# Performance work log

Measured on AMD Instinct MI355X. Metric: run time of the kernel, lower is better.

Reference implementation:

```python
import jax, jax.numpy as jnp
import numpy as np

N = 50000
IN_F = 256
HID = 32
HEADS = 4
NEG_SLOPE = 0.2


def _gat_layer(x, edge_index, W, a_src, a_dst, bias):
    # x: [N, Fin]; W: [Fin, H*C]; a_src/a_dst: [H, C]; bias: [H*C]
    n = x.shape[0]
    H, C = a_src.shape
    h = (x @ W).reshape(n, H, C)                     # [N, H, C]
    alpha_src = jnp.einsum('nhc,hc->nh', h, a_src)   # [N, H]
    alpha_dst = jnp.einsum('nhc,hc->nh', h, a_dst)   # [N, H]
    src, dst = edge_index[0], edge_index[1]
    logits = alpha_src[src] + alpha_dst[dst]         # [E, H]
    logits = jax.nn.leaky_relu(logits, negative_slope=NEG_SLOPE)
    # segment softmax over edges grouped by destination node
    seg_max = jax.ops.segment_max(logits, dst, num_segments=n)
    seg_max = jnp.where(jnp.isfinite(seg_max), seg_max, 0.0)
    e = jnp.exp(logits - seg_max[dst])               # [E, H]
    denom = jax.ops.segment_sum(e, dst, num_segments=n)  # [N, H]
    attn = e / (denom[dst] + 1e-16)                  # [E, H]
    msg = h[src] * attn[:, :, None]                  # [E, H, C]
    out = jax.ops.segment_sum(msg, dst, num_segments=n)  # [N, H, C]
    return out.reshape(n, H * C) + bias


def _add_self_loops(edge_index, n):
    # PyG GATConv default add_self_loops=True
    loops = jnp.arange(n, dtype=edge_index.dtype)
    return jnp.concatenate([edge_index, jnp.stack([loops, loops])], axis=1)


def setup_inputs() -> dict:
    key = jax.random.key(0)
    ks = jax.random.split(key, 10)
    x = jax.random.normal(ks[0], (N, IN_F), dtype=jnp.float32)
    edge_index = jax.random.randint(ks[1], (2, 800000), 0, N, dtype=jnp.int64)
    d1 = HEADS * HID
    s1 = 1.0 / np.sqrt(IN_F)
    W1 = jax.random.normal(ks[2], (IN_F, d1), dtype=jnp.float32) * s1
    a_src1 = jax.random.normal(ks[3], (HEADS, HID), dtype=jnp.float32) * 0.1
    a_dst1 = jax.random.normal(ks[4], (HEADS, HID), dtype=jnp.float32) * 0.1
    b1 = jnp.zeros((d1,), dtype=jnp.float32)
    s2 = 1.0 / np.sqrt(d1)
    W2 = jax.random.normal(ks[5], (d1, d1), dtype=jnp.float32) * s2
    a_src2 = jax.random.normal(ks[6], (HEADS, HID), dtype=jnp.float32) * 0.1
    a_dst2 = jax.random.normal(ks[7], (HEADS, HID), dtype=jnp.float32) * 0.1
    b2 = jnp.zeros((d1,), dtype=jnp.float32)
    return {"x": x, "edge_index": edge_index, "W1": W1, "a_src1": a_src1,
            "a_dst1": a_dst1, "b1": b1, "W2": W2, "a_src2": a_src2,
            "a_dst2": a_dst2, "b2": b2}


def reference(x, edge_index, W1, a_src1, a_dst1, b1, W2, a_src2, a_dst2, b2):
    # Inference mode: dropout layers are identity.
    ei = _add_self_loops(edge_index, x.shape[0])
    h = _gat_layer(x, ei, W1, a_src1, a_dst1, b1)
    h = jax.nn.elu(h)
    h = _gat_layer(h, ei, W2, a_src2, a_dst2, b2)
    return h
```

## Files before the change

### kernel.cpp

```cpp
#include <hip/hip_runtime.h>
#include <hip/hip_fp16.h>
#include <math.h>

#define HEADS 4
#define HID 32
#define D1 128
#define IN_FEAT 256
#define NEG_SLOPE 0.2f
#define CAP 64
#define AGG_NODES 8
#define EPT 8

#define WTS_STRIDE_H 72
#define HTS_STRIDE_H 136
#define SMEM_BYTES (128 * 272)

typedef _Float16 half8 __attribute__((ext_vector_type(8)));
typedef float f32x4 __attribute__((ext_vector_type(4)));
typedef long long ll2 __attribute__((ext_vector_type(2)));

static inline int ceil_div(int a, int b) { return (a + b - 1) / b; }

static __device__ inline float2 unpack_h2(unsigned int v) {
    __half2 h = __builtin_bit_cast(__half2, v);
    return __half22float2(h);
}

static __device__ inline void fma_mix_lo(float& a, unsigned int h2, float w) {
    asm("v_fma_mix_f32 %0, %1, %2, %0 op_sel:[0,0,0] op_sel_hi:[1,0,0]"
        : "+v"(a) : "v"(h2), "v"(w));
}
static __device__ inline void fma_mix_hi(float& a, unsigned int h2, float w) {
    asm("v_fma_mix_f32 %0, %1, %2, %0 op_sel:[1,0,0] op_sel_hi:[1,0,0]"
        : "+v"(a) : "v"(h2), "v"(w));
}

__global__ void init_prep(const unsigned int* __restrict__ raw, int* __restrict__ flag,
                          const float* __restrict__ W1, _Float16* __restrict__ WT1,
                          const float* __restrict__ W2, _Float16* __restrict__ WT2,
                          int* __restrict__ cnt, int N) {
    int i = blockIdx.x * blockDim.x + threadIdx.x;
    if (i < N) cnt[i] = 0;
    if (i < IN_FEAT * D1) {
        int k = i >> 7, n = i & 127;
        WT1[(size_t)n * IN_FEAT + k] = (_Float16)W1[i];
    }
    if (i < D1 * D1) {
        int k = i >> 7, n = i & 127;
        WT2[(size_t)n * D1 + k] = (_Float16)W2[i];
    }
    if (blockIdx.x == 0 && threadIdx.x < 64) {
        unsigned int hi = raw[2 * threadIdx.x + 1];
        unsigned long long b = __ballot(hi != 0u);
        if (threadIdx.x == 0) *flag = (b == 0ULL) ? 1 : 0;
    }
}

__device__ void scatter_body(int sbid, const void* __restrict__ raw,
                             const int* __restrict__ flag,
                             int* __restrict__ cnt,
                             unsigned short* __restrict__ slots,
                             int E) {
    const int e0 = (sbid * 256 + (int)threadIdx.x) * EPT;
    if (e0 >= E) return;
    const bool wide = (*flag != 0);
    int s[EPT], d[EPT];
    if (e0 + EPT <= E) {
        if (wide) {
            const ll2* ps = (const ll2*)((const long long*)raw + e0);
            const ll2* pd = (const ll2*)((const long long*)raw + E + e0);
#pragma unroll
            for (int i = 0; i < EPT / 2; ++i) {
                ll2 a = ps[i], b = pd[i];
                s[2 * i] = (int)a[0]; s[2 * i + 1] = (int)a[1];
                d[2 * i] = (int)b[0]; d[2 * i + 1] = (int)b[1];
            }
        } else {
            const int4* ps = (const int4*)((const int*)raw + e0);
            const int4* pd = (const int4*)((const int*)raw + E + e0);
#pragma unroll
            for (int i = 0; i < EPT / 4; ++i) {
                int4 a = ps[i], b = pd[i];
                s[4 * i] = a.x; s[4 * i + 1] = a.y; s[4 * i + 2] = a.z; s[4 * i + 3] = a.w;
                d[4 * i] = b.x; d[4 * i + 1] = b.y; d[4 * i + 2] = b.z; d[4 * i + 3] = b.w;
            }
        }
        int p[EPT];
#pragma unroll
        for (int i = 0; i < EPT; ++i) p[i] = atomicAdd(&cnt[d[i]], 1);
#pragma unroll
        for (int i = 0; i < EPT; ++i)
            if (p[i] < CAP) slots[(size_t)d[i] * CAP + p[i]] = (unsigned short)s[i];
    } else {
        for (int e = e0; e < E; ++e) {
            int ss, dd;
            if (wide) { ss = (int)((const long long*)raw)[e]; dd = (int)((const long long*)raw)[E + e]; }
            else      { ss = ((const int*)raw)[e];            dd = ((const int*)raw)[E + e]; }
            int p = atomicAdd(&cnt[dd], 1);
            if (p < CAP) slots[(size_t)dd * CAP + p] = (unsigned short)ss;
        }
    }
}

template <int AF16>
__device__ void gemm_body(char* smem, int bid, const void* __restrict__ Ain,
                          const _Float16* __restrict__ WT,
                          _Float16* __restrict__ Hout,
                          const float* __restrict__ a_src,
                          const float* __restrict__ a_dst,
                          float* __restrict__ asrc_out,
                          float* __restrict__ adst_out,
                          int M, int K) {
    const int tid = threadIdx.x;
    const int wave = tid >> 6, lane = tid & 63;
    const int quad = lane >> 4, l16 = lane & 15;
    const int row0 = bid * 128;
    const int m0 = min(row0 + wave * 32 + l16, M - 1);
    const int m1 = min(row0 + wave * 32 + 16 + l16, M - 1);
    const float*    Af = (const float*)Ain;
    const _Float16* Ah = (const _Float16*)Ain;
    const uint4* WTg = (const uint4*)WT;
    const int K8 = K >> 3;

    f32x4 acc[2][8];
#pragma unroll
    for (int r = 0; r < 2; ++r)
#pragma unroll
        for (int c = 0; c < 8; ++c) acc[r][c] = (f32x4){0.f, 0.f, 0.f, 0.f};

    for (int kb = 0; kb < K; kb += 64) {
        __syncthreads();
#pragma unroll
        for (int i = 0; i < 4; ++i) {
            int c = tid + i * 256;
            int n = c >> 3, j = c & 7;
            uint4 v = WTg[(size_t)n * K8 + (kb >> 3) + j];
            *(uint4*)(smem + n * 144 + j * 16) = v;
        }
        __syncthreads();
#pragma unroll
        for (int kc = 0; kc < 2; ++kc) {
            int k0 = kb + kc * 32 + quad * 8;
            half8 a0f, a1f;
            if (AF16) {
                a0f = *(const half8*)(Ah + (size_t)m0 * K + k0);
                a1f = *(const half8*)(Ah + (size_t)m1 * K + k0);
            } else {
                float4 x0 = *(const float4*)(Af + (size_t)m0 * K + k0);
                float4 x1 = *(const float4*)(Af + (size_t)m0 * K + k0 + 4);
                float4 y0 = *(const float4*)(Af + (size_t)m1 * K + k0);
                float4 y1 = *(const float4*)(Af + (size_t)m1 * K + k0 + 4);
                a0f[0] = (_Float16)x0.x; a0f[1] = (_Float16)x0.y;
                a0f[2] = (_Float16)x0.z; a0f[3] = (_Float16)x0.w;
                a0f[4] = (_Float16)x1.x; a0f[5] = (_Float16)x1.y;
                a0f[6] = (_Float16)x1.z; a0f[7] = (_Float16)x1.w;
                a1f[0] = (_Float16)y0.x; a1f[1] = (_Float16)y0.y;
                a1f[2] = (_Float16)y0.z; a1f[3] = (_Float16)y0.w;
                a1f[4] = (_Float16)y1.x; a1f[5] = (_Float16)y1.y;
                a1f[6] = (_Float16)y1.z; a1f[7] = (_Float16)y1.w;
            }
#pragma unroll
            for (int c = 0; c < 8; ++c) {
                half8 bf = *(const half8*)(smem + (c * 16 + l16) * 144 + kc * 64 + quad * 16);
                acc[0][c] = __builtin_amdgcn_mfma_f32_16x16x32_f16(a0f, bf, acc[0][c], 0, 0, 0);
                acc[1][c] = __builtin_amdgcn_mfma_f32_16x16x32_f16(a1f, bf, acc[1][c], 0, 0, 0);
            }
        }
    }

    __syncthreads();
    _Float16* hts = (_Float16*)smem;
#pragma unroll
    for (int r = 0; r < 2; ++r)
#pragma unroll
        for (int c = 0; c < 8; ++c)
#pragma unroll
            for (int g = 0; g < 4; ++g) {
                int row = wave * 32 + r * 16 + quad * 4 + g;
                hts[row * HTS_STRIDE_H + c * 16 + l16] = (_Float16)acc[r][c][g];
            }
    __syncthreads();

    const int r = tid >> 1;
    const int part = tid & 1;
    const int grow = row0 + r;
    const uint4* hrow = (const uint4*)(smem + r * 272 + part * 128);
    if (grow < M) {
        uint4* dv = (uint4*)(Hout + (size_t)grow * 128 + part * 64);
#pragma unroll
        for (int i = 0; i < 8; ++i) dv[i] = hrow[i];
    }
#pragma unroll
    for (int t = 0; t < 2; ++t) {
        int hh = part * 2 + t;
        const uint4* hv = (const uint4*)(smem + r * 272 + hh * 64);
        const float4* as4 = (const float4*)(a_src + hh * HID);
        const float4* ad4 = (const float4*)(a_dst + hh * HID);
        float ps = 0.f, pd = 0.f;
#pragma unroll
        for (int b = 0; b < 4; ++b) {
            uint4 u = hv[b];
            float2 f0 = unpack_h2(u.x), f1 = unpack_h2(u.y);
            float2 f2 = unpack_h2(u.z), f3 = unpack_h2(u.w);
            float4 s0 = as4[b * 2], s1 = as4[b * 2 + 1];
            float4 d0 = ad4[b * 2], d1 = ad4[b * 2 + 1];
            ps += f0.x * s0.x + f0.y * s0.y + f1.x * s0.z + f1.y * s0.w
                + f2.x * s1.x + f2.y * s1.y + f3.x * s1.z + f3.y * s1.w;
            pd += f0.x * d0.x + f0.y * d0.y + f1.x * d0.z + f1.y * d0.w
                + f2.x * d1.x + f2.y * d1.y + f3.x * d1.z + f3.y * d1.w;
        }
        if (grow < M) {
            asrc_out[grow * 4 + hh] = ps;
            adst_out[grow * 4 + hh] = pd;
        }
    }
}

template <int AF16>
__global__ __launch_bounds__(256) void gemm128(const void* __restrict__ Ain,
                                               const _Float16* __restrict__ WT,
                                               _Float16* __restrict__ Hout,
                                               const float* __restrict__ a_src,
                                               const float* __restrict__ a_dst,
                                               float* __restrict__ asrc_out,
                                               float* __restrict__ adst_out,
                                               int M, int K) {
    __shared__ __align__(16) char smem[SMEM_BYTES];
    gemm_body<AF16>(smem, blockIdx.x, Ain, WT, Hout, a_src, a_dst,
                    asrc_out, adst_out, M, K);
}

template <int AF16>
__global__ __launch_bounds__(256) void gemm128_scatter(const void* __restrict__ Ain,
                                                       const _Float16* __restrict__ WT,
                                                       _Float16* __restrict__ Hout,
                                                       const float* __restrict__ a_src,
                                                       const float* __restrict__ a_dst,
                                                       float* __restrict__ asrc_out,
                                                       float* __restrict__ adst_out,
                                                       int M, int K,
                                                       const void* __restrict__ raw,
                                                       const int* __restrict__ flag,
                                                       int* __restrict__ cnt,
                                                       unsigned short* __restrict__ slots,
                                                       int E, int Sg) {
    __shared__ __align__(16) char smem[SMEM_BYTES];
    if ((int)blockIdx.x < Sg) {
        scatter_body(blockIdx.x, raw, flag, cnt, slots, E);
        return;
    }
    gemm_body<AF16>(smem, blockIdx.x - Sg, Ain, WT, Hout, a_src, a_dst,
                    asrc_out, adst_out, M, K);
}

__global__ __launch_bounds__(256) void aggregate(const _Float16* __restrict__ hb,
                                                 const int* __restrict__ cnt,
                                                 const unsigned short* __restrict__ slots,
                                                 const float* __restrict__ asrc,
                                                 const float* __restrict__ adst,
                                                 const float* __restrict__ bias,
                                                 float* __restrict__ out32,
                                                 _Float16* __restrict__ out16,
                                                 int N, int apply_elu) {
    const int w = threadIdx.x >> 6;
    const int lane = threadIdx.x & 63;
    const int half = lane >> 5;
    const int hl = lane & 31;
    const int idx = w * 2 + half;
    const int node = blockIdx.x * AGG_NODES + idx;
    const bool live = (node < N);

    __shared__ float wsh[AGG_NODES][CAP][4];
    __shared__ int ssh[AGG_NODES][CAP];

    int cntE = 0, count = 1;
    if (live) {
        cntE = min(cnt[node], CAP - 1);
        count = cntE + 1;
    }
    const unsigned short* nslots = slots + (size_t)node * CAP;

    float4 ad4 = live ? *(const float4*)&adst[node * 4] : make_float4(0.f, 0.f, 0.f, 0.f);

    const bool v0 = live && (hl < count);
    const bool v1 = live && (hl + 32 < count);
    float lv0[4] = {-1e30f, -1e30f, -1e30f, -1e30f};
    float lv1[4] = {-1e30f, -1e30f, -1e30f, -1e30f};
    if (v0) {
        int src = (hl < cntE) ? (int)nslots[hl] : node;
        ssh[idx][hl] = src << 8;
        float4 as4 = *(const float4*)&asrc[src * 4];
        float t0 = as4.x + ad4.x, t1 = as4.y + ad4.y;
        float t2 = as4.z + ad4.z, t3 = as4.w + ad4.w;
        lv0[0] = t0 > 0.f ? t0 : NEG_SLOPE * t0;
        lv0[1] = t1 > 0.f ? t1 : NEG_SLOPE * t1;
        lv0[2] = t2 > 0.f ? t2 : NEG_SLOPE * t2;
        lv0[3] = t3 > 0.f ? t3 : NEG_SLOPE * t3;
    }
    if (v1) {
        int j = hl + 32;
        int src = (j < cntE) ? (int)nslots[j] : node;
        ssh[idx][j] = src << 8;
        float4 as4 = *(const float4*)&asrc[src * 4];
        float t0 = as4.x + ad4.x, t1 = as4.y + ad4.y;
        float t2 = as4.z + ad4.z, t3 = as4.w + ad4.w;
        lv1[0] = t0 > 0.f ? t0 : NEG_SLOPE * t0;
        lv1[1] = t1 > 0.f ? t1 : NEG_SLOPE * t1;
        lv1[2] = t2 > 0.f ? t2 : NEG_SLOPE * t2;
        lv1[3] = t3 > 0.f ? t3 : NEG_SLOPE * t3;
    }

    float m[4];
#pragma unroll
    for (int h = 0; h < 4; ++h) m[h] = fmaxf(lv0[h], lv1[h]);
#pragma unroll
    for (int off = 16; off >= 1; off >>= 1)
#pragma unroll
        for (int h = 0; h < 4; ++h)
            m[h] = fmaxf(m[h], __shfl_xor(m[h], off, 64));

    float e0[4], e1[4], sum[4];
#pragma unroll
    for (int h = 0; h < 4; ++h) {
        e0[h] = v0 ? __expf(lv0[h] - m[h]) : 0.f;
        e1[h] = v1 ? __expf(lv1[h] - m[h]) : 0.f;
        sum[h] = e0[h] + e1[h];
    }
#pragma unroll
    for (int off = 16; off >= 1; off >>= 1)
#pragma unroll
        for (int h = 0; h < 4; ++h)
            sum[h] += __shfl_xor(sum[h], off, 64);

    if (v0) {
        float4 w4;
        w4.x = e0[0] / (sum[0] + 1e-16f);
        w4.y = e0[1] / (sum[1] + 1e-16f);
        w4.z = e0[2] / (sum[2] + 1e-16f);
        w4.w = e0[3] / (sum[3] + 1e-16f);
        *(float4*)&wsh[idx][hl][0] = w4;
    }
    if (v1) {
        float4 w4;
        w4.x = e1[0] / (sum[0] + 1e-16f);
        w4.y = e1[1] / (sum[1] + 1e-16f);
        w4.z = e1[2] / (sum[2] + 1e-16f);
        w4.w = e1[3] / (sum[3] + 1e-16f);
        *(float4*)&wsh[idx][hl + 32][0] = w4;
    }
    __syncthreads();

    const int q = hl >> 4;
    const int sub = hl & 15;
    const int hh = sub >> 2;
    const char* hbase = (const char*)hb;
    const int sub16 = sub * 16;

    float acc[8];
#pragma unroll
    for (int i = 0; i < 8; ++i) acc[i] = 0.f;

#define LDROW(off) (*(const uint4*)(hbase + (unsigned)((off) + sub16)))
#define ROW_FMA(u, wt)                                   \
    do {                                                 \
        fma_mix_lo(acc[0], (u).x, (wt));                 \
        fma_mix_hi(acc[1], (u).x, (wt));                 \
        fma_mix_lo(acc[2], (u).y, (wt));                 \
        fma_mix_hi(acc[3], (u).y, (wt));                 \
        fma_mix_lo(acc[4], (u).z, (wt));                 \
        fma_mix_hi(acc[5], (u).z, (wt));                 \
        fma_mix_lo(acc[6], (u).w, (wt));                 \
        fma_mix_hi(acc[7], (u).w, (wt));                 \
    } while (0)

    if (live) {
        int j = q;
        if (j + 6 < count) {
            int o0 = ssh[idx][j], o1 = ssh[idx][j + 2], o2 = ssh[idx][j + 4], o3 = ssh[idx][j + 6];
            float w0 = wsh[idx][j][hh], w1 = wsh[idx][j + 2][hh];
            float w2 = wsh[idx][j + 4][hh], w3 = wsh[idx][j + 6][hh];
            uint4 u0 = LDROW(o0), u1 = LDROW(o1), u2 = LDROW(o2), u3 = LDROW(o3);
            for (j += 8; j + 6 < count; j += 8) {
                int p0 = ssh[idx][j], p1 = ssh[idx][j + 2], p2 = ssh[idx][j + 4], p3 = ssh[idx][j + 6];
                float x0 = wsh[idx][j][hh], x1 = wsh[idx][j + 2][hh];
                float x2 = wsh[idx][j + 4][hh], x3 = wsh[idx][j + 6][hh];
                uint4 n0 = LDROW(p0), n1 = LDROW(p1), n2 = LDROW(p2), n3 = LDROW(p3);
                ROW_FMA(u0, w0); ROW_FMA(u1, w1); ROW_FMA(u2, w2); ROW_FMA(u3, w3);
                u0 = n0; u1 = n1; u2 = n2; u3 = n3;
                w0 = x0; w1 = x1; w2 = x2; w3 = x3;
            }
            const bool b0 = j < count, b1 = j + 2 < count, b2 = j + 4 < count;
            uint4 t0 = {0, 0, 0, 0}, t1 = {0, 0, 0, 0}, t2 = {0, 0, 0, 0};
            float y0 = 0.f, y1 = 0.f, y2 = 0.f;
            if (b0) { t0 = LDROW(ssh[idx][j]);     y0 = wsh[idx][j][hh]; }
            if (b1) { t1 = LDROW(ssh[idx][j + 2]); y1 = wsh[idx][j + 2][hh]; }
            if (b2) { t2 = LDROW(ssh[idx][j + 4]); y2 = wsh[idx][j + 4][hh]; }
            ROW_FMA(u0, w0); ROW_FMA(u1, w1); ROW_FMA(u2, w2); ROW_FMA(u3, w3);
            if (b0) ROW_FMA(t0, y0);
            if (b1) ROW_FMA(t1, y1);
            if (b2) ROW_FMA(t2, y2);
        } else {
            const bool b0 = j < count, b1 = j + 2 < count, b2 = j + 4 < count;
            uint4 t0 = {0, 0, 0, 0}, t1 = {0, 0, 0, 0}, t2 = {0, 0, 0, 0};
            float y0 = 0.f, y1 = 0.f, y2 = 0.f;
            if (b0) { t0 = LDROW(ssh[idx][j]);     y0 = wsh[idx][j][hh]; }
            if (b1) { t1 = LDROW(ssh[idx][j + 2]); y1 = wsh[idx][j + 2][hh]; }
            if (b2) { t2 = LDROW(ssh[idx][j + 4]); y2 = wsh[idx][j + 4][hh]; }
            if (b0) ROW_FMA(t0, y0);
            if (b1) ROW_FMA(t1, y1);
            if (b2) ROW_FMA(t2, y2);
        }
    }
#undef ROW_FMA
#undef LDROW

#pragma unroll
    for (int i = 0; i < 8; ++i) acc[i] += __shfl_xor(acc[i], 16, 64);

    if (live && q == 0) {
        int ch8 = sub * 8;
        float o[8];
#pragma unroll
        for (int i = 0; i < 8; ++i) o[i] = acc[i] + bias[ch8 + i];
        if (apply_elu) {
#pragma unroll
            for (int i = 0; i < 8; ++i) o[i] = o[i] > 0.f ? o[i] : __expf(o[i]) - 1.f;
        }
        if (out16) {
            __align__(16) _Float16 t[8];
#pragma unroll
            for (int i = 0; i < 8; ++i) t[i] = (_Float16)o[i];
            *(uint4*)&out16[(size_t)node * D1 + ch8] = *(const uint4*)t;
        } else {
            *(float4*)&out32[(size_t)node * D1 + ch8]     = make_float4(o[0], o[1], o[2], o[3]);
            *(float4*)&out32[(size_t)node * D1 + ch8 + 4] = make_float4(o[4], o[5], o[6], o[7]);
        }
    }
}

extern "C" void kernel_launch(void* const* d_in, const int* in_sizes, int n_in,
                              void* d_out, int out_size, void* d_ws, size_t ws_size,
                              hipStream_t stream) {
    const float* x      = (const float*)d_in[0];
    const void*  e_raw  = d_in[1];
    const float* W1     = (const float*)d_in[2];
    const float* a_src1 = (const float*)d_in[3];
    const float* a_dst1 = (const float*)d_in[4];
    const float* b1     = (const float*)d_in[5];
    const float* W2     = (const float*)d_in[6];
    const float* a_src2 = (const float*)d_in[7];
    const float* a_dst2 = (const float*)d_in[8];
    const float* b2     = (const float*)d_in[9];

    const int N  = in_sizes[0] / IN_FEAT;
    const int E  = in_sizes[1] / 2;
    float* out = (float*)d_out;

    char* ws = (char*)d_ws;
    size_t woff = 0;
    auto walloc = [&](size_t bytes) -> char* {
        char* p = ws + woff;
        woff = (woff + bytes + 255) & ~(size_t)255;
        return p;
    };
    int*   flag  = (int*)walloc(4);
    int*   cnt   = (int*)walloc((size_t)N * 4);
    unsigned short* slots = (unsigned short*)walloc((size_t)N * CAP * 2);
    float* asrc  = (float*)walloc((size_t)N * HEADS * 4);
    float* adst  = (float*)walloc((size_t)N * HEADS * 4);
    _Float16* hb  = (_Float16*)walloc((size_t)N * D1 * 2);
    _Float16* o16 = (_Float16*)walloc((size_t)N * D1 * 2);
    _Float16* WT1 = (_Float16*)walloc((size_t)IN_FEAT * D1 * 2);
    _Float16* WT2 = (_Float16*)walloc((size_t)D1 * D1 * 2);

    const int Gg = ceil_div(N, 128);
    const int Sg = ceil_div(E, 256 * EPT);
    const int Ga = ceil_div(N, AGG_NODES);
    const int initN = (N > IN_FEAT * D1) ? N : IN_FEAT * D1;

    init_prep<<<ceil_div(initN, 256), 256, 0, stream>>>(
        (const unsigned int*)e_raw, flag, W1, WT1, W2, WT2, cnt, N);
    gemm128_scatter<0><<<Sg + Gg, 256, 0, stream>>>(
        x, WT1, hb, a_src1, a_dst1, asrc, adst, N, IN_FEAT,
        e_raw, flag, cnt, slots, E, Sg);
    aggregate<<<Ga, 256, 0, stream>>>(hb, cnt, slots, asrc, adst, b1, nullptr, o16, N, 1);
    gemm128<1><<<Gg, 256, 0, stream>>>(o16, WT2, hb, a_src2, a_dst2, asrc, adst, N, D1);
    aggregate<<<Ga, 256, 0, stream>>>(hb, cnt, slots, asrc, adst, b2, out, nullptr, N, 0);
}
```

Baseline: 244.2 us.

## Fuse all GAT stages into one persistent cooperative kernel with grid syncs

Replaces the five separate kernel launches (init, gemm+scatter, aggregate, gemm, aggregate) with a single persistent cooperative kernel that loops over virtual blocks and separates stages with grid-wide syncs. The goal is to remove launch overhead and inter-kernel gaps. The cost is that grid size is capped by occupancy, so each stage runs as grid-stride loops with one shared-memory allocation sized for the GEMM. Grid barriers add their own cost. The previous multi-launch path is kept as a fallback if the cooperative launch fails.

```diff
diff --git a/kernel.cpp b/kernel.cpp
--- a/kernel.cpp
+++ b/kernel.cpp
@@ -1,6 +1,9 @@
 #include <hip/hip_runtime.h>
 #include <hip/hip_fp16.h>
+#include <hip/hip_cooperative_groups.h>
 #include <math.h>
+
+namespace cg = cooperative_groups;
 
 #define HEADS 4
 #define HID 32
@@ -14,6 +17,7 @@
 #define WTS_STRIDE_H 72
 #define HTS_STRIDE_H 136
 #define SMEM_BYTES (128 * 272)
+#define AGG_SMEM (AGG_NODES * CAP * 4 * 4 + AGG_NODES * CAP * 4)
 
 typedef _Float16 half8 __attribute__((ext_vector_type(8)));
 typedef float f32x4 __attribute__((ext_vector_type(4)));
@@ -33,27 +37,6 @@
 static __device__ inline void fma_mix_hi(float& a, unsigned int h2, float w) {
     asm("v_fma_mix_f32 %0, %1, %2, %0 op_sel:[1,0,0] op_sel_hi:[1,0,0]"
         : "+v"(a) : "v"(h2), "v"(w));
-}
-
-__global__ void init_prep(const unsigned int* __restrict__ raw, int* __restrict__ flag,
-                          const float* __restrict__ W1, _Float16* __restrict__ WT1,
-                          const float* __restrict__ W2, _Float16* __restrict__ WT2,
-                          int* __restrict__ cnt, int N) {
-    int i = blockIdx.x * blockDim.x + threadIdx.x;
-    if (i < N) cnt[i] = 0;
-    if (i < IN_FEAT * D1) {
-        int k = i >> 7, n = i & 127;
-        WT1[(size_t)n * IN_FEAT + k] = (_Float16)W1[i];
-    }
-    if (i < D1 * D1) {
-        int k = i >> 7, n = i & 127;
-        WT2[(size_t)n * D1 + k] = (_Float16)W2[i];
-    }
-    if (blockIdx.x == 0 && threadIdx.x < 64) {
-        unsigned int hi = raw[2 * threadIdx.x + 1];
-        unsigned long long b = __ballot(hi != 0u);
-        if (threadIdx.x == 0) *flag = (b == 0ULL) ? 1 : 0;
-    }
 }
 
 __device__ void scatter_body(int sbid, const void* __restrict__ raw,
@@ -216,62 +199,26 @@
     }
 }
 
-template <int AF16>
-__global__ __launch_bounds__(256) void gemm128(const void* __restrict__ Ain,
-                                               const _Float16* __restrict__ WT,
-                                               _Float16* __restrict__ Hout,
-                                               const float* __restrict__ a_src,
-                                               const float* __restrict__ a_dst,
-                                               float* __restrict__ asrc_out,
-                                               float* __restrict__ adst_out,
-                                               int M, int K) {
-    __shared__ __align__(16) char smem[SMEM_BYTES];
-    gemm_body<AF16>(smem, blockIdx.x, Ain, WT, Hout, a_src, a_dst,
-                    asrc_out, adst_out, M, K);
-}
-
-template <int AF16>
-__global__ __launch_bounds__(256) void gemm128_scatter(const void* __restrict__ Ain,
-                                                       const _Float16* __restrict__ WT,
-                                                       _Float16* __restrict__ Hout,
-                                                       const float* __restrict__ a_src,
-                                                       const float* __restrict__ a_dst,
-                                                       float* __restrict__ asrc_out,
-                                                       float* __restrict__ adst_out,
-                                                       int M, int K,
-                                                       const void* __restrict__ raw,
-                                                       const int* __restrict__ flag,
-                                                       int* __restrict__ cnt,
-                                                       unsigned short* __restrict__ slots,
-                                                       int E, int Sg) {
-    __shared__ __align__(16) char smem[SMEM_BYTES];
-    if ((int)blockIdx.x < Sg) {
-        scatter_body(blockIdx.x, raw, flag, cnt, slots, E);
-        return;
-    }
-    gemm_body<AF16>(smem, blockIdx.x - Sg, Ain, WT, Hout, a_src, a_dst,
-                    asrc_out, adst_out, M, K);
-}
-
-__global__ __launch_bounds__(256) void aggregate(const _Float16* __restrict__ hb,
-                                                 const int* __restrict__ cnt,
-                                                 const unsigned short* __restrict__ slots,
-                                                 const float* __restrict__ asrc,
-                                                 const float* __restrict__ adst,
-                                                 const float* __restrict__ bias,
-                                                 float* __restrict__ out32,
-                                                 _Float16* __restrict__ out16,
-                                                 int N, int apply_elu) {
+__device__ void agg_body(char* smem_, int bid,
+                         const _Float16* __restrict__ hb,
+                         const int* __restrict__ cnt,
+                         const unsigned short* __restrict__ slots,
+                         const float* __restrict__ asrc,
+                         const float* __restrict__ adst,
+                         const float* __restrict__ bias,
+                         float* __restrict__ out32,
+                         _Float16* __restrict__ out16,
+                         int N, int apply_elu) {
+    float (*wsh)[CAP][4] = (float (*)[CAP][4])smem_;
+    int (*ssh)[CAP] = (int (*)[CAP])(smem_ + AGG_NODES * CAP * 4 * sizeof(float));
+
     const int w = threadIdx.x >> 6;
     const int lane = threadIdx.x & 63;
     const int half = lane >> 5;
     const int hl = lane & 31;
     const int idx = w * 2 + half;
-    const int node = blockIdx.x * AGG_NODES + idx;
+    const int node = bid * AGG_NODES + idx;
     const bool live = (node < N);
-
-    __shared__ float wsh[AGG_NODES][CAP][4];
-    __shared__ int ssh[AGG_NODES][CAP];
 
     int cntE = 0, count = 1;
     if (live) {
@@ -436,6 +383,133 @@
             *(float4*)&out32[(size_t)node * D1 + ch8 + 4] = make_float4(o[4], o[5], o[6], o[7]);
         }
     }
+    __syncthreads();
+}
+
+struct MegaArgs {
+    const void* x; const void* e_raw;
+    const float *W1, *as1, *ad1, *b1, *W2, *as2, *ad2, *b2;
+    int* flag; int* cnt; unsigned short* slots;
+    float *asrc, *adst;
+    _Float16 *hb, *o16, *WT1, *WT2;
+    float* out;
+    int N, E, initN, Sg, Gg, Ga;
+};
+
+__global__ __launch_bounds__(256) void mega(MegaArgs a) {
+    __shared__ __align__(16) char smem[SMEM_BYTES];
+    cg::grid_group grid = cg::this_grid();
+
+    for (int i = blockIdx.x * 256 + (int)threadIdx.x; i < a.initN; i += gridDim.x * 256) {
+        if (i < a.N) a.cnt[i] = 0;
+        if (i < IN_FEAT * D1) {
+            int k = i >> 7, n = i & 127;
+            a.WT1[(size_t)n * IN_FEAT + k] = (_Float16)a.W1[i];
+        }
+        if (i < D1 * D1) {
+            int k = i >> 7, n = i & 127;
+            a.WT2[(size_t)n * D1 + k] = (_Float16)a.W2[i];
+        }
+    }
+    if (blockIdx.x == 0 && threadIdx.x < 64) {
+        unsigned int hi = ((const unsigned int*)a.e_raw)[2 * threadIdx.x + 1];
+        unsigned long long b = __ballot(hi != 0u);
+        if (threadIdx.x == 0) *a.flag = (b == 0ULL) ? 1 : 0;
+    }
+    grid.sync();
+
+    for (int vb = blockIdx.x; vb < a.Sg + a.Gg; vb += gridDim.x) {
+        if (vb < a.Sg) scatter_body(vb, a.e_raw, a.flag, a.cnt, a.slots, a.E);
+        else gemm_body<0>(smem, vb - a.Sg, a.x, a.WT1, a.hb, a.as1, a.ad1,
+                          a.asrc, a.adst, a.N, IN_FEAT);
+    }
+    grid.sync();
+
+    for (int vb = blockIdx.x; vb < a.Ga; vb += gridDim.x)
+        agg_body(smem, vb, a.hb, a.cnt, a.slots, a.asrc, a.adst, a.b1,
+                 nullptr, a.o16, a.N, 1);
+    grid.sync();
+
+    for (int vb = blockIdx.x; vb < a.Gg; vb += gridDim.x)
+        gemm_body<1>(smem, vb, a.o16, a.WT2, a.hb, a.as2, a.ad2,
+                     a.asrc, a.adst, a.N, D1);
+    grid.sync();
+
+    for (int vb = blockIdx.x; vb < a.Ga; vb += gridDim.x)
+        agg_body(smem, vb, a.hb, a.cnt, a.slots, a.asrc, a.adst, a.b2,
+                 a.out, nullptr, a.N, 0);
+}
+
+__global__ void init_prep(const unsigned int* __restrict__ raw, int* __restrict__ flag,
+                          const float* __restrict__ W1, _Float16* __restrict__ WT1,
+                          const float* __restrict__ W2, _Float16* __restrict__ WT2,
+                          int* __restrict__ cnt, int N) {
+    int i = blockIdx.x * blockDim.x + threadIdx.x;
+    if (i < N) cnt[i] = 0;
+    if (i < IN_FEAT * D1) {
+        int k = i >> 7, n = i & 127;
+        WT1[(size_t)n * IN_FEAT + k] = (_Float16)W1[i];
+    }
+    if (i < D1 * D1) {
+        int k = i >> 7, n = i & 127;
+        WT2[(size_t)n * D1 + k] = (_Float16)W2[i];
+    }
+    if (blockIdx.x == 0 && threadIdx.x < 64) {
+        unsigned int hi = raw[2 * threadIdx.x + 1];
+        unsigned long long b = __ballot(hi != 0u);
+        if (threadIdx.x == 0) *flag = (b == 0ULL) ? 1 : 0;
+    }
+}
+
+template <int AF16>
+__global__ __launch_bounds__(256) void gemm128(const void* __restrict__ Ain,
+                                               const _Float16* __restrict__ WT,
+                                               _Float16* __restrict__ Hout,
+                                               const float* __restrict__ a_src,
+                                               const float* __restrict__ a_dst,
+                                               float* __restrict__ asrc_out,
+                                               float* __restrict__ adst_out,
+                                               int M, int K) {
+    __shared__ __align__(16) char smem[SMEM_BYTES];
+    gemm_body<AF16>(smem, blockIdx.x, Ain, WT, Hout, a_src, a_dst,
+                    asrc_out, adst_out, M, K);
+}
+
+template <int AF16>
+__global__ __launch_bounds__(256) void gemm128_scatter(const void* __restrict__ Ain,
+                                                       const _Float16* __restrict__ WT,
+                                                       _Float16* __restrict__ Hout,
+                                                       const float* __restrict__ a_src,
+                                                       const float* __restrict__ a_dst,
+                                                       float* __restrict__ asrc_out,
+                                                       float* __restrict__ adst_out,
+                                                       int M, int K,
+                                                       const void* __restrict__ raw,
+                                                       const int* __restrict__ flag,
+                                                       int* __restrict__ cnt,
+                                                       unsigned short* __restrict__ slots,
+                                                       int E, int Sg) {
+    __shared__ __align__(16) char smem[SMEM_BYTES];
+    if ((int)blockIdx.x < Sg) {
+        scatter_body(blockIdx.x, raw, flag, cnt, slots, E);
+        return;
+    }
+    gemm_body<AF16>(smem, blockIdx.x - Sg, Ain, WT, Hout, a_src, a_dst,
+                    asrc_out, adst_out, M, K);
+}
+
+__global__ __launch_bounds__(256) void aggregate(const _Float16* __restrict__ hb,
+                                                 const int* __restrict__ cnt,
+                                                 const unsigned short* __restrict__ slots,
+                                                 const float* __restrict__ asrc,
+                                                 const float* __restrict__ adst,
+                                                 const float* __restrict__ bias,
+                                                 float* __restrict__ out32,
+                                                 _Float16* __restrict__ out16,
+                                                 int N, int apply_elu) {
+    __shared__ __align__(16) char smem[AGG_SMEM];
+    agg_body(smem, blockIdx.x, hb, cnt, slots, asrc, adst, bias,
+             out32, out16, N, apply_elu);
 }
 
 extern "C" void kernel_launch(void* const* d_in, const int* in_sizes, int n_in,
@@ -478,12 +552,50 @@
     const int Ga = ceil_div(N, AGG_NODES);
     const int initN = (N > IN_FEAT * D1) ? N : IN_FEAT * D1;
 
-    init_prep<<<ceil_div(initN, 256), 256, 0, stream>>>(
-        (const unsigned int*)e_raw, flag, W1, WT1, W2, WT2, cnt, N);
-    gemm128_scatter<0><<<Sg + Gg, 256, 0, stream>>>(
-        x, WT1, hb, a_src1, a_dst1, asrc, adst, N, IN_FEAT,
-        e_raw, flag, cnt, slots, E, Sg);
-    aggregate<<<Ga, 256, 0, stream>>>(hb, cnt, slots, asrc, adst, b1, nullptr, o16, N, 1);
-    gemm128<1><<<Gg, 256, 0, stream>>>(o16, WT2, hb, a_src2, a_dst2, asrc, adst, N, D1);
-    aggregate<<<Ga, 256, 0, stream>>>(hb, cnt, slots, asrc, adst, b2, out, nullptr, N, 0);
-}
+    static int g_grid = -2;
+    if (g_grid == -2) {
+        int nb = 0;
+        hipError_t e = hipOccupancyMaxActiveBlocksPerMultiprocessor(&nb, mega, 256, 0);
+        if (e == hipSuccess && nb > 0) {
+            int dev = 0, ncu = 0;
+            hipGetDevice(&dev);
+            hipDeviceGetAttribute(&ncu, hipDeviceAttributeMultiprocessorCount, dev);
+            g_grid = (ncu > 0) ? nb * ncu : 0;
+        } else {
+            g_grid = 0;
+        }
+    }
+
+    bool done = false;
+    if (g_grid > 0) {
+        MegaArgs ma;
+        ma.x = x; ma.e_raw = e_raw;
+        ma.W1 = W1; ma.as1 = a_src1; ma.ad1 = a_dst1; ma.b1 = b1;
+        ma.W2 = W2; ma.as2 = a_src2; ma.ad2 = a_dst2; ma.b2 = b2;
+        ma.flag = flag; ma.cnt = cnt; ma.slots = slots;
+        ma.asrc = asrc; ma.adst = adst;
+        ma.hb = hb; ma.o16 = o16; ma.WT1 = WT1; ma.WT2 = WT2;
+        ma.out = out;
+        ma.N = N; ma.E = E; ma.initN = initN;
+        ma.Sg = Sg; ma.Gg = Gg; ma.Ga = Ga;
+        void* params[] = { &ma };
+        hipError_t err = hipLaunchCooperativeKernel(mega, dim3(g_grid), dim3(256),
+                                                    params, 0, stream);
+        done = (err == hipSuccess);
+        if (!done) g_grid = 0;
+    }
+
+    if (!done) {
+        init_prep<<<ceil_div(initN, 256), 256, 0, stream>>>(
+            (const unsigned int*)e_raw, flag, W1, WT1, W2, WT2, cnt, N);
+        gemm128_scatter<0><<<Sg + Gg, 256, 0, stream>>>(
+            x, WT1, hb, a_src1, a_dst1, asrc, adst, N, IN_FEAT,
+            e_raw, flag, cnt, slots, E, Sg);
+        aggregate<<<Ga, 256, 0, stream>>>(hb, cnt, slots, asrc, adst, b1,
+                                          nullptr, o16, N, 1);
+        gemm128<1><<<Gg, 256, 0, stream>>>(o16, WT2, hb, a_src2, a_dst2,
+                                           asrc, adst, N, D1);
+        aggregate<<<Ga, 256, 0, stream>>>(hb, cnt, slots, asrc, adst, b2,
+                                          out, nullptr, N, 0);
+    }
+}
```

After: 281.1 us. +15.1%, slower.

## Split aggregation across heads with one block per head per node group

Applied to the files above, without the earlier changes.

The aggregation kernel now assigns each block a single attention head for a group of 8 nodes, with block indices interleaved so that 8 consecutive blocks cover 4 heads and 2 node groups. Each lane computes only one head's softmax weight, and the gather loads only that head's 64-byte slice of each neighbour row, with 8 edges processed in parallel per 4-lane group. This is meant to raise parallelism and shrink per-thread work. In exchange, the softmax logits and slot indices are recomputed 4 times per node and neighbour rows are fetched in four separate pieces, relying on L2 locality across the interleaved blocks.

```diff
diff --git a/kernel.cpp b/kernel.cpp
--- a/kernel.cpp
+++ b/kernel.cpp
@@ -8,7 +8,7 @@
 #define IN_FEAT 256
 #define NEG_SLOPE 0.2f
 #define CAP 64
-#define AGG_NODES 8
+#define HS_NODES 8
 #define EPT 8
 
 #define WTS_STRIDE_H 72
@@ -253,25 +253,31 @@
                     asrc_out, adst_out, M, K);
 }
 
-__global__ __launch_bounds__(256) void aggregate(const _Float16* __restrict__ hb,
-                                                 const int* __restrict__ cnt,
-                                                 const unsigned short* __restrict__ slots,
-                                                 const float* __restrict__ asrc,
-                                                 const float* __restrict__ adst,
-                                                 const float* __restrict__ bias,
-                                                 float* __restrict__ out32,
-                                                 _Float16* __restrict__ out16,
-                                                 int N, int apply_elu) {
-    const int w = threadIdx.x >> 6;
+__global__ __launch_bounds__(256) void aggregate_hs(const _Float16* __restrict__ hb,
+                                                    const int* __restrict__ cnt,
+                                                    const unsigned short* __restrict__ slots,
+                                                    const float* __restrict__ asrc,
+                                                    const float* __restrict__ adst,
+                                                    const float* __restrict__ bias,
+                                                    float* __restrict__ out32,
+                                                    _Float16* __restrict__ out16,
+                                                    int N, int apply_elu, int NB) {
+    const int x    = blockIdx.x & 7;
+    const int g    = blockIdx.x >> 3;
+    const int head = x >> 1;
+    const int nb   = g * 2 + (x & 1);
+    if (nb >= NB) return;
+
+    const int wv = threadIdx.x >> 6;
     const int lane = threadIdx.x & 63;
     const int half = lane >> 5;
     const int hl = lane & 31;
-    const int idx = w * 2 + half;
-    const int node = blockIdx.x * AGG_NODES + idx;
+    const int idx = wv * 2 + half;
+    const int node = nb * HS_NODES + idx;
     const bool live = (node < N);
 
-    __shared__ float wsh[AGG_NODES][CAP][4];
-    __shared__ int ssh[AGG_NODES][CAP];
+    __shared__ float wsh[HS_NODES][CAP];
+    __shared__ int ssh[HS_NODES][CAP];
 
     int cntE = 0, count = 1;
     if (live) {
@@ -279,88 +285,51 @@
         count = cntE + 1;
     }
     const unsigned short* nslots = slots + (size_t)node * CAP;
-
-    float4 ad4 = live ? *(const float4*)&adst[node * 4] : make_float4(0.f, 0.f, 0.f, 0.f);
+    const float adh = live ? adst[node * 4 + head] : 0.f;
+    const int hoff = head * 64;
 
     const bool v0 = live && (hl < count);
     const bool v1 = live && (hl + 32 < count);
-    float lv0[4] = {-1e30f, -1e30f, -1e30f, -1e30f};
-    float lv1[4] = {-1e30f, -1e30f, -1e30f, -1e30f};
+    float lv0 = -1e30f, lv1 = -1e30f;
     if (v0) {
         int src = (hl < cntE) ? (int)nslots[hl] : node;
-        ssh[idx][hl] = src << 8;
-        float4 as4 = *(const float4*)&asrc[src * 4];
-        float t0 = as4.x + ad4.x, t1 = as4.y + ad4.y;
-        float t2 = as4.z + ad4.z, t3 = as4.w + ad4.w;
-        lv0[0] = t0 > 0.f ? t0 : NEG_SLOPE * t0;
-        lv0[1] = t1 > 0.f ? t1 : NEG_SLOPE * t1;
-        lv0[2] = t2 > 0.f ? t2 : NEG_SLOPE * t2;
-        lv0[3] = t3 > 0.f ? t3 : NEG_SLOPE * t3;
+        ssh[idx][hl] = (src << 8) + hoff;
+        float t = asrc[src * 4 + head] + adh;
+        lv0 = t > 0.f ? t : NEG_SLOPE * t;
     }
     if (v1) {
         int j = hl + 32;
         int src = (j < cntE) ? (int)nslots[j] : node;
-        ssh[idx][j] = src << 8;
-        float4 as4 = *(const float4*)&asrc[src * 4];
-        float t0 = as4.x + ad4.x, t1 = as4.y + ad4.y;
-        float t2 = as4.z + ad4.z, t3 = as4.w + ad4.w;
-        lv1[0] = t0 > 0.f ? t0 : NEG_SLOPE * t0;
-        lv1[1] = t1 > 0.f ? t1 : NEG_SLOPE * t1;
-        lv1[2] = t2 > 0.f ? t2 : NEG_SLOPE * t2;
-        lv1[3] = t3 > 0.f ? t3 : NEG_SLOPE * t3;
-    }
-
-    float m[4];
-#pragma unroll
-    for (int h = 0; h < 4; ++h) m[h] = fmaxf(lv0[h], lv1[h]);
+        ssh[idx][j] = (src << 8) + hoff;
+        float t = asrc[src * 4 + head] + adh;
+        lv1 = t > 0.f ? t : NEG_SLOPE * t;
+    }
+
+    float m = fmaxf(lv0, lv1);
 #pragma unroll
     for (int off = 16; off >= 1; off >>= 1)
-#pragma unroll
-        for (int h = 0; h < 4; ++h)
-            m[h] = fmaxf(m[h], __shfl_xor(m[h], off, 64));
-
-    float e0[4], e1[4], sum[4];
-#pragma unroll
-    for (int h = 0; h < 4; ++h) {
-        e0[h] = v0 ? __expf(lv0[h] - m[h]) : 0.f;
-        e1[h] = v1 ? __expf(lv1[h] - m[h]) : 0.f;
-        sum[h] = e0[h] + e1[h];
-    }
+        m = fmaxf(m, __shfl_xor(m, off, 64));
+    float e0 = v0 ? __expf(lv0 - m) : 0.f;
+    float e1 = v1 ? __expf(lv1 - m) : 0.f;
+    float sum = e0 + e1;
 #pragma unroll
     for (int off = 16; off >= 1; off >>= 1)
-#pragma unroll
-        for (int h = 0; h < 4; ++h)
-            sum[h] += __shfl_xor(sum[h], off, 64);
-
-    if (v0) {
-        float4 w4;
-        w4.x = e0[0] / (sum[0] + 1e-16f);
-        w4.y = e0[1] / (sum[1] + 1e-16f);
-        w4.z = e0[2] / (sum[2] + 1e-16f);
-        w4.w = e0[3] / (sum[3] + 1e-16f);
-        *(float4*)&wsh[idx][hl][0] = w4;
-    }
-    if (v1) {
-        float4 w4;
-        w4.x = e1[0] / (sum[0] + 1e-16f);
-        w4.y = e1[1] / (sum[1] + 1e-16f);
-        w4.z = e1[2] / (sum[2] + 1e-16f);
-        w4.w = e1[3] / (sum[3] + 1e-16f);
-        *(float4*)&wsh[idx][hl + 32][0] = w4;
-    }
+        sum += __shfl_xor(sum, off, 64);
+    float inv = 1.f / (sum + 1e-16f);
+    if (v0) wsh[idx][hl] = e0 * inv;
+    if (v1) wsh[idx][hl + 32] = e1 * inv;
     __syncthreads();
 
-    const int q = hl >> 4;
-    const int sub = hl & 15;
-    const int hh = sub >> 2;
+    const int e8 = hl >> 2;
+    const int s4 = hl & 3;
     const char* hbase = (const char*)hb;
-    const int sub16 = sub * 16;
+    const int s16 = s4 * 16;
 
     float acc[8];
 #pragma unroll
     for (int i = 0; i < 8; ++i) acc[i] = 0.f;
 
-#define LDROW(off) (*(const uint4*)(hbase + (unsigned)((off) + sub16)))
+#define LDROW(off) (*(const uint4*)(hbase + (unsigned)((off) + s16)))
 #define ROW_FMA(u, wt)                                   \
     do {                                                 \
         fma_mix_lo(acc[0], (u).x, (wt));                 \
@@ -374,54 +343,40 @@
     } while (0)
 
     if (live) {
-        int j = q;
-        if (j + 6 < count) {
-            int o0 = ssh[idx][j], o1 = ssh[idx][j + 2], o2 = ssh[idx][j + 4], o3 = ssh[idx][j + 6];
-            float w0 = wsh[idx][j][hh], w1 = wsh[idx][j + 2][hh];
-            float w2 = wsh[idx][j + 4][hh], w3 = wsh[idx][j + 6][hh];
-            uint4 u0 = LDROW(o0), u1 = LDROW(o1), u2 = LDROW(o2), u3 = LDROW(o3);
-            for (j += 8; j + 6 < count; j += 8) {
-                int p0 = ssh[idx][j], p1 = ssh[idx][j + 2], p2 = ssh[idx][j + 4], p3 = ssh[idx][j + 6];
-                float x0 = wsh[idx][j][hh], x1 = wsh[idx][j + 2][hh];
-                float x2 = wsh[idx][j + 4][hh], x3 = wsh[idx][j + 6][hh];
-                uint4 n0 = LDROW(p0), n1 = LDROW(p1), n2 = LDROW(p2), n3 = LDROW(p3);
-                ROW_FMA(u0, w0); ROW_FMA(u1, w1); ROW_FMA(u2, w2); ROW_FMA(u3, w3);
-                u0 = n0; u1 = n1; u2 = n2; u3 = n3;
-                w0 = x0; w1 = x1; w2 = x2; w3 = x3;
-            }
-            const bool b0 = j < count, b1 = j + 2 < count, b2 = j + 4 < count;
-            uint4 t0 = {0, 0, 0, 0}, t1 = {0, 0, 0, 0}, t2 = {0, 0, 0, 0};
-            float y0 = 0.f, y1 = 0.f, y2 = 0.f;
-            if (b0) { t0 = LDROW(ssh[idx][j]);     y0 = wsh[idx][j][hh]; }
-            if (b1) { t1 = LDROW(ssh[idx][j + 2]); y1 = wsh[idx][j + 2][hh]; }
-            if (b2) { t2 = LDROW(ssh[idx][j + 4]); y2 = wsh[idx][j + 4][hh]; }
-            ROW_FMA(u0, w0); ROW_FMA(u1, w1); ROW_FMA(u2, w2); ROW_FMA(u3, w3);
-            if (b0) ROW_FMA(t0, y0);
-            if (b1) ROW_FMA(t1, y1);
-            if (b2) ROW_FMA(t2, y2);
-        } else {
-            const bool b0 = j < count, b1 = j + 2 < count, b2 = j + 4 < count;
-            uint4 t0 = {0, 0, 0, 0}, t1 = {0, 0, 0, 0}, t2 = {0, 0, 0, 0};
-            float y0 = 0.f, y1 = 0.f, y2 = 0.f;
-            if (b0) { t0 = LDROW(ssh[idx][j]);     y0 = wsh[idx][j][hh]; }
-            if (b1) { t1 = LDROW(ssh[idx][j + 2]); y1 = wsh[idx][j + 2][hh]; }
-            if (b2) { t2 = LDROW(ssh[idx][j + 4]); y2 = wsh[idx][j + 4][hh]; }
-            if (b0) ROW_FMA(t0, y0);
-            if (b1) ROW_FMA(t1, y1);
-            if (b2) ROW_FMA(t2, y2);
+        int j = e8;
+        bool b0 = j < count, b1 = (j + 8) < count;
+        uint4 u0 = {0, 0, 0, 0}, u1 = {0, 0, 0, 0};
+        float w0 = 0.f, w1 = 0.f;
+        if (b0) { u0 = LDROW(ssh[idx][j]);     w0 = wsh[idx][j]; }
+        if (b1) { u1 = LDROW(ssh[idx][j + 8]); w1 = wsh[idx][j + 8]; }
+        j += 16;
+        while (b0) {
+            bool n0 = j < count, n1 = (j + 8) < count;
+            uint4 v0u = {0, 0, 0, 0}, v1u = {0, 0, 0, 0};
+            float x0 = 0.f, x1 = 0.f;
+            if (n0) { v0u = LDROW(ssh[idx][j]);     x0 = wsh[idx][j]; }
+            if (n1) { v1u = LDROW(ssh[idx][j + 8]); x1 = wsh[idx][j + 8]; }
+            ROW_FMA(u0, w0);
+            if (b1) ROW_FMA(u1, w1);
+            u0 = v0u; u1 = v1u; w0 = x0; w1 = x1; b0 = n0; b1 = n1;
+            j += 16;
         }
     }
 #undef ROW_FMA
 #undef LDROW
 
 #pragma unroll
-    for (int i = 0; i < 8; ++i) acc[i] += __shfl_xor(acc[i], 16, 64);
-
-    if (live && q == 0) {
-        int ch8 = sub * 8;
+    for (int i = 0; i < 8; ++i) {
+        acc[i] += __shfl_xor(acc[i], 4, 64);
+        acc[i] += __shfl_xor(acc[i], 8, 64);
+        acc[i] += __shfl_xor(acc[i], 16, 64);
+    }
+
+    if (live && e8 == 0) {
+        const int ch0 = head * HID + s4 * 8;
         float o[8];
 #pragma unroll
-        for (int i = 0; i < 8; ++i) o[i] = acc[i] + bias[ch8 + i];
+        for (int i = 0; i < 8; ++i) o[i] = acc[i] + bias[ch0 + i];
         if (apply_elu) {
 #pragma unroll
             for (int i = 0; i < 8; ++i) o[i] = o[i] > 0.f ? o[i] : __expf(o[i]) - 1.f;
@@ -430,10 +385,10 @@
             __align__(16) _Float16 t[8];
 #pragma unroll
             for (int i = 0; i < 8; ++i) t[i] = (_Float16)o[i];
-            *(uint4*)&out16[(size_t)node * D1 + ch8] = *(const uint4*)t;
+            *(uint4*)&out16[(size_t)node * D1 + ch0] = *(const uint4*)t;
         } else {
-            *(float4*)&out32[(size_t)node * D1 + ch8]     = make_float4(o[0], o[1], o[2], o[3]);
-            *(float4*)&out32[(size_t)node * D1 + ch8 + 4] = make_float4(o[4], o[5], o[6], o[7]);
+            *(float4*)&out32[(size_t)node * D1 + ch0]     = make_float4(o[0], o[1], o[2], o[3]);
+            *(float4*)&out32[(size_t)node * D1 + ch0 + 4] = make_float4(o[4], o[5], o[6], o[7]);
         }
     }
 }
@@ -475,7 +430,8 @@
 
     const int Gg = ceil_div(N, 128);
     const int Sg = ceil_div(E, 256 * EPT);
-    const int Ga = ceil_div(N, AGG_NODES);
+    const int NB = ceil_div(N, HS_NODES);
+    const int Ghs = ceil_div(NB, 2) * 8;
     const int initN = (N > IN_FEAT * D1) ? N : IN_FEAT * D1;
 
     init_prep<<<ceil_div(initN, 256), 256, 0, stream>>>(
@@ -483,7 +439,10 @@
     gemm128_scatter<0><<<Sg + Gg, 256, 0, stream>>>(
         x, WT1, hb, a_src1, a_dst1, asrc, adst, N, IN_FEAT,
         e_raw, flag, cnt, slots, E, Sg);
-    aggregate<<<Ga, 256, 0, stream>>>(hb, cnt, slots, asrc, adst, b1, nullptr, o16, N, 1);
-    gemm128<1><<<Gg, 256, 0, stream>>>(o16, WT2, hb, a_src2, a_dst2, asrc, adst, N, D1);
-    aggregate<<<Ga, 256, 0, stream>>>(hb, cnt, slots, asrc, adst, b2, out, nullptr, N, 0);
-}
+    aggregate_hs<<<Ghs, 256, 0, stream>>>(hb, cnt, slots, asrc, adst, b1,
+                                          nullptr, o16, N, 1, NB);
+    gemm128<1><<<Gg, 256, 0, stream>>>(o16, WT2, hb, a_src2, a_dst2,
+                                       asrc, adst, N, D1);
+    aggregate_hs<<<Ghs, 256, 0, stream>>>(hb, cnt, slots, asrc, adst, b2,
+                                          out, nullptr, N, 0, NB);
+}
```

Measured after the change: 291.2 us. 19.2% more time.
